# Optimization experiments

Measured on AMD Instinct MI355X. Metric: run time of the kernel, lower is better.

The kernel has to match this reference:

```python
import jax, jax.numpy as jnp
import numpy as np

D_MODEL = 1024
D_FF = 4096
N_EXPERTS = 8
TOP_K = 2
GATE_TEMP = 1.0
LOAD_BALANCE_WEIGHT = 0.01


def setup_inputs() -> dict:
    key = jax.random.key(0)
    ks = jax.random.split(key, 6)
    B, S = 4, 2048
    x = jax.random.normal(ks[0], (B, S, D_MODEL), dtype=jnp.float32)
    # gate: nn.Linear(d_model, n_experts, bias=False), weight ~ N(0, 0.1)
    gate_w = 0.1 * jax.random.normal(ks[1], (N_EXPERTS, D_MODEL), dtype=jnp.float32)
    # stacked expert weights (stored as [in, out] for x @ W)
    s1 = 1.0 / np.sqrt(D_MODEL)
    s2 = 1.0 / np.sqrt(D_FF)
    W1 = jax.random.uniform(ks[2], (N_EXPERTS, D_MODEL, D_FF), jnp.float32, -s1, s1)
    b1 = jax.random.uniform(ks[3], (N_EXPERTS, D_FF), jnp.float32, -s1, s1)
    W2 = jax.random.uniform(ks[4], (N_EXPERTS, D_FF, D_MODEL), jnp.float32, -s2, s2)
    b2 = jax.random.uniform(ks[5], (N_EXPERTS, D_MODEL), jnp.float32, -s2, s2)
    return {"x": x, "gate_w": gate_w, "W1": W1, "b1": b1, "W2": W2, "b2": b2}


def reference(x, gate_w, W1, b1, W2, b2):
    B, S, D = x.shape
    E = gate_w.shape[0]
    xf = x.reshape(-1, D)                                  # [N, D]
    logits = (xf @ gate_w.T) / GATE_TEMP                   # [N, E]
    gate_probs = jax.nn.softmax(logits, axis=-1)           # [N, E]
    topk_probs, topk_idx = jax.lax.top_k(gate_probs, TOP_K)
    topk_probs = topk_probs / jnp.sum(topk_probs, axis=-1, keepdims=True)
    # per-token combine weight for each expert: [N, E]
    combine = jnp.einsum("nk,nke->ne", topk_probs,
                         jax.nn.one_hot(topk_idx, E, dtype=xf.dtype))
    out = jnp.zeros_like(xf)
    for e in range(E):  # fixed small loop over experts (structurally distinct weights)
        h = jax.nn.gelu(xf @ W1[e] + b1[e], approximate=False)  # [N, d_ff]
        out = out + combine[:, e:e + 1] * (h @ W2[e] + b2[e])
    out = out.reshape(B, S, D)
    # auxiliary load-balance loss (faithful: softmax probs > 0 almost surely)
    prob_mean = jnp.mean(gate_probs, axis=0)
    tokens_per_expert = jnp.mean((gate_probs > 0).astype(xf.dtype), axis=0)
    aux_loss = jnp.sum(prob_mean * tokens_per_expert) * E * LOAD_BALANCE_WEIGHT
    return out, aux_loss
```

## Files before the change

### kernel.cpp

```cpp
#include <hip/hip_runtime.h>
#include <cstdint>

typedef unsigned short u16;
typedef __attribute__((ext_vector_type(8))) __bf16 bf16x8;
typedef __attribute__((ext_vector_type(4))) float f32x4;

#define NTOK 8192
#define DM   1024
#define DFF  4096
#define NE   8
#define NT_MAX 136

typedef const __attribute__((address_space(1))) unsigned gl_u32;
typedef __attribute__((address_space(3))) unsigned lds_u32;

static __device__ __forceinline__ u16 f2bf(float f) {
    union { float f; unsigned u; } v; v.f = f;
    unsigned r = v.u + 0x7fffu + ((v.u >> 16) & 1u);
    return (u16)(r >> 16);
}

__global__ __launch_bounds__(256) void transpose_cvt_kernel(const float* __restrict__ W,
                                                            u16* __restrict__ WT,
                                                            int K, int F) {
    __shared__ float tile[32][33];
    size_t eo = (size_t)blockIdx.z * K * F;
    const float* src = W + eo;
    u16* dst = WT + eo;
    int f0 = blockIdx.x * 32, k0 = blockIdx.y * 32;
    int c = threadIdx.x & 31, r0 = threadIdx.x >> 5;
#pragma unroll
    for (int r = r0; r < 32; r += 8)
        tile[r][c] = src[(size_t)(k0 + r) * F + f0 + c];
    __syncthreads();
#pragma unroll
    for (int r = r0; r < 32; r += 8)
        dst[(size_t)(f0 + r) * K + k0 + c] = f2bf(tile[c][r]);
}

__global__ __launch_bounds__(256) void gate_kernel(const float* __restrict__ x,
                                                   const float* __restrict__ gw,
                                                   u16* __restrict__ xb,
                                                   int* __restrict__ cnt,
                                                   float* __restrict__ psum,
                                                   float* __restrict__ indsum,
                                                   int* __restrict__ list,
                                                   float* __restrict__ wgt,
                                                   int4* __restrict__ tokIE,
                                                   float2* __restrict__ tokW) {
    __shared__ float s_psum[NE], s_ind[NE];
    __shared__ int s_cnt[NE], s_base[NE];
    __shared__ int s_tok[NE][32];
    __shared__ float s_wgt[NE][32];
    __shared__ int s_e1[32], s_p1[32], s_e2[32], s_p2[32];
    __shared__ float s_w1[32], s_w2[32];
    int tid = threadIdx.x, lane = tid & 63, wid = tid >> 6;
    if (tid < NE) { s_psum[tid] = 0.f; s_ind[tid] = 0.f; s_cnt[tid] = 0; }
    __syncthreads();
#pragma unroll 1
    for (int it = 0; it < 8; it++) {
        int t = blockIdx.x * 32 + wid * 8 + it;
        const float* xr = x + (size_t)t * DM;
        float xv[16];
#pragma unroll
        for (int i = 0; i < 4; i++) {
            f32x4 v = *(const f32x4*)(xr + i * 256 + lane * 4);
            xv[4 * i + 0] = v[0]; xv[4 * i + 1] = v[1];
            xv[4 * i + 2] = v[2]; xv[4 * i + 3] = v[3];
            ushort4 o;
            o.x = f2bf(v[0]); o.y = f2bf(v[1]); o.z = f2bf(v[2]); o.w = f2bf(v[3]);
            *(ushort4*)(xb + (size_t)t * DM + i * 256 + lane * 4) = o;
        }
        float p[NE];
#pragma unroll
        for (int e = 0; e < NE; e++) {
            const float* gr = gw + (size_t)e * DM;
            float d = 0.f;
#pragma unroll
            for (int i = 0; i < 4; i++) {
                f32x4 g = *(const f32x4*)(gr + i * 256 + lane * 4);
                d += xv[4 * i] * g[0] + xv[4 * i + 1] * g[1]
                   + xv[4 * i + 2] * g[2] + xv[4 * i + 3] * g[3];
            }
#pragma unroll
            for (int off = 32; off; off >>= 1) d += __shfl_xor(d, off);
            p[e] = d;
        }
        float m = p[0];
#pragma unroll
        for (int e = 1; e < NE; e++) m = fmaxf(m, p[e]);
        float s = 0.f;
#pragma unroll
        for (int e = 0; e < NE; e++) { p[e] = expf(p[e] - m); s += p[e]; }
        float inv = 1.f / s;
#pragma unroll
        for (int e = 0; e < NE; e++) p[e] *= inv;
        int i1 = 0; float p1 = p[0];
#pragma unroll
        for (int e = 1; e < NE; e++) if (p[e] > p1) { p1 = p[e]; i1 = e; }
        int i2 = (i1 == 0) ? 1 : 0; float p2 = p[i2];
#pragma unroll
        for (int e = 0; e < NE; e++) if (e != i1 && p[e] > p2) { p2 = p[e]; i2 = e; }
        float wnorm = 1.f / (p1 + p2);
        if (lane == 0) {
#pragma unroll
            for (int e = 0; e < NE; e++) {
                atomicAdd(&s_psum[e], p[e]);
                atomicAdd(&s_ind[e], (p[e] > 0.f) ? 1.f : 0.f);
            }
            int pos1 = atomicAdd(&s_cnt[i1], 1);
            s_tok[i1][pos1] = t; s_wgt[i1][pos1] = p1 * wnorm;
            int pos2 = atomicAdd(&s_cnt[i2], 1);
            s_tok[i2][pos2] = t; s_wgt[i2][pos2] = p2 * wnorm;
            int sl = wid * 8 + it;
            s_e1[sl] = i1; s_p1[sl] = pos1; s_w1[sl] = p1 * wnorm;
            s_e2[sl] = i2; s_p2[sl] = pos2; s_w2[sl] = p2 * wnorm;
        }
    }
    __syncthreads();
    if (tid < NE) {
        s_base[tid] = atomicAdd(&cnt[tid], s_cnt[tid]);
        atomicAdd(&psum[tid], s_psum[tid]);
        atomicAdd(&indsum[tid], s_ind[tid]);
    }
    __syncthreads();
    for (int idx = tid; idx < NE * 32; idx += 256) {
        int e = idx >> 5, j = idx & 31;
        if (j < s_cnt[e]) {
            list[e * NTOK + s_base[e] + j] = s_tok[e][j];
            wgt[e * NTOK + s_base[e] + j] = s_wgt[e][j];
        }
    }
    if (tid < 32) {
        int t = blockIdx.x * 32 + tid;
        int e1 = s_e1[tid], e2 = s_e2[tid];
        tokIE[t] = make_int4(e1, s_base[e1] + s_p1[tid], e2, s_base[e2] + s_p2[tid]);
        tokW[t] = make_float2(s_w1[tid], s_w2[tid]);
    }
}

__global__ void finalize_kernel(const float* __restrict__ psum,
                                const float* __restrict__ indsum,
                                const int* __restrict__ cnt,
                                int* __restrict__ baseArr,
                                int* __restrict__ tileE,
                                int* __restrict__ tileM0,
                                int* __restrict__ nTiles,
                                float* __restrict__ out_aux) {
    if (threadIdx.x == 0) {
        float a = 0.f; int b = 0, nt = 0;
        for (int e = 0; e < NE; e++) {
            a += (psum[e] * (1.f / NTOK)) * (indsum[e] * (1.f / NTOK));
            baseArr[e] = b; b += cnt[e];
            int mt = (cnt[e] + 127) >> 7;
            for (int i = 0; i < mt; i++) { tileE[nt] = e; tileM0[nt] = i; nt++; }
        }
        nTiles[0] = nt;
        out_aux[0] = a * (float)NE * 0.01f;
    }
}

template <int KDIM, int EPI>
__global__ __launch_bounds__(256, 4) void gemm_kernel(const u16* __restrict__ A,
                                                      const u16* __restrict__ BT,
                                                      const float* __restrict__ bias,
                                                      const int* __restrict__ list,
                                                      const float* __restrict__ wgt,
                                                      const int* __restrict__ cnt,
                                                      const int* __restrict__ base,
                                                      const int* __restrict__ tileE,
                                                      const int* __restrict__ tileM0,
                                                      const int* __restrict__ nTiles,
                                                      u16* __restrict__ h_out,
                                                      float* __restrict__ out) {
    constexpr int NCOL = (EPI == 1) ? DFF : DM;
    constexpr int NY = NCOL / 128;
    constexpr int NT = KDIM / 64;
    constexpr int BAND = 4 * NY;
    int nwg = gridDim.x;
    int q = nwg >> 3, r = nwg & 7;
    int xcd = blockIdx.x & 7, idx0 = blockIdx.x >> 3;
    int wg = (xcd < r ? xcd * (q + 1) : r * (q + 1) + (xcd - r) * q) + idx0;
    int band = wg / BAND, ib = wg - band * BAND;
    int ny = ib >> 2;
    int t = band * 4 + (ib & 3);
    if (t >= nTiles[0]) return;
    int e = tileE[t];
    int m0 = tileM0[t] << 7;
    int M = cnt[e];
    int hb = base[e];
    int n0 = ny * 128;
    const int* le = list + e * NTOK;
    const float* we = wgt + e * NTOK;
    const u16* Bte = BT + (size_t)e * NCOL * KDIM;
    const float* be = bias + (size_t)e * NCOL;

    __shared__ __attribute__((aligned(16))) u16 lA[128 * 64];
    __shared__ __attribute__((aligned(16))) u16 lB[128 * 64];

    int tid = threadIdx.x;
    int lane = tid & 63, wid = tid >> 6;
    int wr = wid >> 1, wc = wid & 1;
    int r16 = lane & 15, hi = lane >> 4;
    int r8 = r16 & 7;

    const u16* aG[4]; const u16* bG[4]; int lofs[4];
#pragma unroll
    for (int qq = 0; qq < 4; qq++) {
        int lin = qq * 256 + tid;
        int row = lin >> 3, j = lin & 7;
        int js = j ^ (row & 7);
        lofs[qq] = lin * 8;
        int pos = m0 + row; if (pos > M - 1) pos = M - 1;
        size_t arow = (EPI == 1) ? (size_t)le[pos] : (size_t)(hb + pos);
        aG[qq] = A + arow * KDIM + js * 8;
        bG[qq] = Bte + (size_t)(n0 + row) * KDIM + js * 8;
    }

#define STAGE(k0)                                                                   \
    do {                                                                            \
        _Pragma("unroll")                                                           \
        for (int qq = 0; qq < 4; qq++) {                                            \
            __builtin_amdgcn_global_load_lds((gl_u32*)(aG[qq] + (k0)),              \
                (lds_u32*)(lA + lofs[qq]), 16, 0, 0);                               \
            __builtin_amdgcn_global_load_lds((gl_u32*)(bG[qq] + (k0)),              \
                (lds_u32*)(lB + lofs[qq]), 16, 0, 0);                               \
        }                                                                           \
    } while (0)

    f32x4 acc[4][4];
#pragma unroll
    for (int m = 0; m < 4; m++)
#pragma unroll
        for (int n = 0; n < 4; n++) acc[m][n] = (f32x4){0.f, 0.f, 0.f, 0.f};

    STAGE(0);

#pragma unroll 1
    for (int tI = 0; tI < NT; ++tI) {
        asm volatile("s_waitcnt vmcnt(0)" ::: "memory");
        __builtin_amdgcn_s_barrier();
#pragma unroll
        for (int kk = 0; kk < 2; kk++) {
            bf16x8 aF[4], bF[4];
            int ch = ((kk << 2) | hi) ^ r8;
#pragma unroll
            for (int m = 0; m < 4; m++)
                aF[m] = *(const bf16x8*)(lA + ((wr * 64 + m * 16 + r16) << 6) + (ch << 3));
#pragma unroll
            for (int n = 0; n < 4; n++)
                bF[n] = *(const bf16x8*)(lB + ((wc * 64 + n * 16 + r16) << 6) + (ch << 3));
            __builtin_amdgcn_s_setprio(1);
#pragma unroll
            for (int m = 0; m < 4; m++)
#pragma unroll
                for (int n = 0; n < 4; n++)
                    acc[m][n] = __builtin_amdgcn_mfma_f32_16x16x32_bf16(aF[m], bF[n], acc[m][n], 0, 0, 0);
            __builtin_amdgcn_s_setprio(0);
        }
        asm volatile("s_waitcnt lgkmcnt(0)" ::: "memory");
        __builtin_amdgcn_s_barrier();
        if (tI + 1 < NT) STAGE((tI + 1) * 64);
    }
#undef STAGE

#pragma unroll
    for (int m = 0; m < 4; m++) {
        int pr = m0 + wr * 64 + m * 16 + hi * 4;
#pragma unroll
        for (int n = 0; n < 4; n++) {
            int f = n0 + wc * 64 + n * 16 + r16;
#pragma unroll
            for (int j = 0; j < 4; j++) {
                int p = pr + j;
                if (p < M) {
                    if constexpr (EPI == 1) {
                        float v = acc[m][n][j] + be[f];
                        float ex = __expf(v * (1.5957691216f + 0.0713548162f * v * v));
                        v = v - v / (ex + 1.0f);
                        h_out[(size_t)(hb + p) * DFF + f] = f2bf(v);
                    } else if constexpr (EPI == 2) {
                        out[(size_t)(hb + p) * DM + f] = acc[m][n][j];
                    } else {
                        atomicAdd(out + (size_t)le[p] * DM + f,
                                  we[p] * (acc[m][n][j] + be[f]));
                    }
                }
            }
        }
    }
}

__global__ __launch_bounds__(256) void combine_kernel(const float* __restrict__ pairOut,
                                                      const float* __restrict__ b2,
                                                      const int4* __restrict__ tokIE,
                                                      const float2* __restrict__ tokW,
                                                      const int* __restrict__ baseArr,
                                                      float* __restrict__ out) {
    int t = blockIdx.x;
    int c = threadIdx.x * 4;
    int4 ie = tokIE[t];
    float2 w = tokW[t];
    int s1 = baseArr[ie.x] + ie.y, s2 = baseArr[ie.z] + ie.w;
    f32x4 v1 = *(const f32x4*)(pairOut + (size_t)s1 * DM + c);
    f32x4 v2 = *(const f32x4*)(pairOut + (size_t)s2 * DM + c);
    f32x4 g1 = *(const f32x4*)(b2 + (size_t)ie.x * DM + c);
    f32x4 g2 = *(const f32x4*)(b2 + (size_t)ie.z * DM + c);
    f32x4 res = w.x * (v1 + g1) + w.y * (v2 + g2);
    *(f32x4*)(out + (size_t)t * DM + c) = res;
}

extern "C" void kernel_launch(void* const* d_in, const int* in_sizes, int n_in,
                              void* d_out, int out_size, void* d_ws, size_t ws_size,
                              hipStream_t stream) {
    const float* x  = (const float*)d_in[0];
    const float* gw = (const float*)d_in[1];
    const float* W1 = (const float*)d_in[2];
    const float* b1 = (const float*)d_in[3];
    const float* W2 = (const float*)d_in[4];
    const float* b2 = (const float*)d_in[5];
    float* out = (float*)d_out;

    char* ws = (char*)d_ws;
    size_t o_xb   = 0;
    size_t o_w1t  = (size_t)16 << 20;
    size_t o_w2t  = o_w1t + ((size_t)64 << 20);
    size_t o_h    = o_w2t + ((size_t)64 << 20);
    size_t o_pair = o_h + ((size_t)128 << 20);
    size_t ctrl_sz = (size_t)1 << 20;
    bool pair_path = ws_size >= o_pair + ((size_t)64 << 20) + ctrl_sz;
    size_t o_ctrl = pair_path ? (o_pair + ((size_t)64 << 20)) : o_pair;

    u16* xb   = (u16*)(ws + o_xb);
    u16* w1t  = (u16*)(ws + o_w1t);
    u16* w2t  = (u16*)(ws + o_w2t);
    u16* h    = (u16*)(ws + o_h);
    float* pairOut = (float*)(ws + o_pair);
    char* ctrl = ws + o_ctrl;
    int*    cnt     = (int*)ctrl;
    float*  psum    = (float*)(ctrl + 32);
    float*  indsum  = (float*)(ctrl + 64);
    int*    baseArr = (int*)(ctrl + 96);
    int*    list    = (int*)(ctrl + 192);
    float*  wgt     = (float*)(ctrl + 192 + 262144);
    int4*   tokIE   = (int4*)(ctrl + 192 + 524288);
    float2* tokW    = (float2*)(ctrl + 192 + 655360);
    int*    tileE   = (int*)(ctrl + 192 + 720896);
    int*    tileM0  = (int*)(ctrl + 192 + 724992);
    int*    nTiles  = (int*)(ctrl + 192 + 729088);

    (void)hipMemsetAsync(ctrl, 0, 192, stream);
    if (!pair_path)
        (void)hipMemsetAsync(d_out, 0, (size_t)out_size * sizeof(float), stream);

    transpose_cvt_kernel<<<dim3(DFF / 32, DM / 32, NE), 256, 0, stream>>>(W1, w1t, DM, DFF);
    transpose_cvt_kernel<<<dim3(DM / 32, DFF / 32, NE), 256, 0, stream>>>(W2, w2t, DFF, DM);
    gate_kernel<<<NTOK / 32, 256, 0, stream>>>(x, gw, xb, cnt, psum, indsum, list, wgt, tokIE, tokW);
    finalize_kernel<<<1, 64, 0, stream>>>(psum, indsum, cnt, baseArr, tileE, tileM0, nTiles,
                                          out + (size_t)NTOK * DM);

    gemm_kernel<DM, 1><<<dim3(NT_MAX * (DFF / 128)), 256, 0, stream>>>(
        xb, w1t, b1, list, wgt, cnt, baseArr, tileE, tileM0, nTiles, h, nullptr);
    if (pair_path) {
        gemm_kernel<DFF, 2><<<dim3(NT_MAX * (DM / 128)), 256, 0, stream>>>(
            h, w2t, b2, list, wgt, cnt, baseArr, tileE, tileM0, nTiles, nullptr, pairOut);
        combine_kernel<<<NTOK, 256, 0, stream>>>(pairOut, b2, tokIE, tokW, baseArr, out);
    } else {
        gemm_kernel<DFF, 3><<<dim3(NT_MAX * (DM / 128)), 256, 0, stream>>>(
            h, w2t, b2, list, wgt, cnt, baseArr, tileE, tileM0, nTiles, nullptr, out);
    }
}
```

Baseline: 572.3 us.

## Grow expert GEMM tiles to 256x128 with 512-thread blocks; vectorize weight transpose

The grouped expert GEMMs now use 256-row M tiles computed by 8 waves of 512 threads. Each B tile loaded into LDS is shared by twice as many rows, which halves weight traffic per output. The tile count per expert and the grid bound are recomputed to match. The weight transpose/convert kernel now reads with float4 vectors and writes 16-byte bf16 chunks on a 64x32 tile. Larger tiles waste more padding rows for experts with ragged counts, and they lower occupancy per CU.

Measured after the change: 572.6 us. Within noise of the previous version (+0.1%).

```diff
diff --git a/kernel.cpp b/kernel.cpp
--- a/kernel.cpp
+++ b/kernel.cpp
@@ -9,7 +9,7 @@
 #define DM   1024
 #define DFF  4096
 #define NE   8
-#define NT_MAX 136
+#define NT_MAX256 72
 
 typedef const __attribute__((address_space(1))) unsigned gl_u32;
 typedef __attribute__((address_space(3))) unsigned lds_u32;
@@ -23,19 +23,31 @@
 __global__ __launch_bounds__(256) void transpose_cvt_kernel(const float* __restrict__ W,
                                                             u16* __restrict__ WT,
                                                             int K, int F) {
-    __shared__ float tile[32][33];
+    __shared__ float tile[64][33];
     size_t eo = (size_t)blockIdx.z * K * F;
     const float* src = W + eo;
     u16* dst = WT + eo;
-    int f0 = blockIdx.x * 32, k0 = blockIdx.y * 32;
-    int c = threadIdx.x & 31, r0 = threadIdx.x >> 5;
-#pragma unroll
-    for (int r = r0; r < 32; r += 8)
-        tile[r][c] = src[(size_t)(k0 + r) * F + f0 + c];
+    int k0 = blockIdx.y * 64, f0 = blockIdx.x * 32;
+    int tid = threadIdx.x;
+    {
+        int rk = tid >> 2, cf = (tid & 3) * 8;
+        const float* s = src + (size_t)(k0 + rk) * F + f0 + cf;
+        f32x4 v0 = *(const f32x4*)(s);
+        f32x4 v1 = *(const f32x4*)(s + 4);
+#pragma unroll
+        for (int i = 0; i < 4; i++) { tile[rk][cf + i] = v0[i]; tile[rk][cf + 4 + i] = v1[i]; }
+    }
     __syncthreads();
-#pragma unroll
-    for (int r = r0; r < 32; r += 8)
-        dst[(size_t)(f0 + r) * K + k0 + c] = f2bf(tile[c][r]);
+    {
+        int f = tid >> 3, kq = (tid & 7) * 8;
+        union { ushort4 h[2]; uint4 q; } o;
+#pragma unroll
+        for (int i = 0; i < 8; i++) {
+            u16 b = f2bf(tile[kq + i][f]);
+            ((u16*)&o)[i] = b;
+        }
+        *(uint4*)(dst + (size_t)(f0 + f) * K + k0 + kq) = o.q;
+    }
 }
 
 __global__ __launch_bounds__(256) void gate_kernel(const float* __restrict__ x,
@@ -152,7 +164,7 @@
         for (int e = 0; e < NE; e++) {
             a += (psum[e] * (1.f / NTOK)) * (indsum[e] * (1.f / NTOK));
             baseArr[e] = b; b += cnt[e];
-            int mt = (cnt[e] + 127) >> 7;
+            int mt = (cnt[e] + 255) >> 8;
             for (int i = 0; i < mt; i++) { tileE[nt] = e; tileM0[nt] = i; nt++; }
         }
         nTiles[0] = nt;
@@ -161,7 +173,7 @@
 }
 
 template <int KDIM, int EPI>
-__global__ __launch_bounds__(256, 4) void gemm_kernel(const u16* __restrict__ A,
+__global__ __launch_bounds__(512, 2) void gemm_kernel(const u16* __restrict__ A,
                                                       const u16* __restrict__ BT,
                                                       const float* __restrict__ bias,
                                                       const int* __restrict__ list,
@@ -186,7 +198,7 @@
     int t = band * 4 + (ib & 3);
     if (t >= nTiles[0]) return;
     int e = tileE[t];
-    int m0 = tileM0[t] << 7;
+    int m0 = tileM0[t] << 8;
     int M = cnt[e];
     int hb = base[e];
     int n0 = ny * 128;
@@ -195,37 +207,45 @@
     const u16* Bte = BT + (size_t)e * NCOL * KDIM;
     const float* be = bias + (size_t)e * NCOL;
 
-    __shared__ __attribute__((aligned(16))) u16 lA[128 * 64];
+    __shared__ __attribute__((aligned(16))) u16 lA[256 * 64];
     __shared__ __attribute__((aligned(16))) u16 lB[128 * 64];
 
     int tid = threadIdx.x;
     int lane = tid & 63, wid = tid >> 6;
-    int wr = wid >> 1, wc = wid & 1;
+    int wm = wid >> 1, wn = wid & 1;
     int r16 = lane & 15, hi = lane >> 4;
     int r8 = r16 & 7;
 
-    const u16* aG[4]; const u16* bG[4]; int lofs[4];
+    const u16* aG[4]; const u16* bG[2]; int aOfs[4], bOfs[2];
 #pragma unroll
     for (int qq = 0; qq < 4; qq++) {
-        int lin = qq * 256 + tid;
+        int lin = qq * 512 + tid;
         int row = lin >> 3, j = lin & 7;
         int js = j ^ (row & 7);
-        lofs[qq] = lin * 8;
+        aOfs[qq] = lin * 8;
         int pos = m0 + row; if (pos > M - 1) pos = M - 1;
         size_t arow = (EPI == 1) ? (size_t)le[pos] : (size_t)(hb + pos);
         aG[qq] = A + arow * KDIM + js * 8;
+    }
+#pragma unroll
+    for (int qq = 0; qq < 2; qq++) {
+        int lin = qq * 512 + tid;
+        int row = lin >> 3, j = lin & 7;
+        int js = j ^ (row & 7);
+        bOfs[qq] = lin * 8;
         bG[qq] = Bte + (size_t)(n0 + row) * KDIM + js * 8;
     }
 
 #define STAGE(k0)                                                                   \
     do {                                                                            \
         _Pragma("unroll")                                                           \
-        for (int qq = 0; qq < 4; qq++) {                                            \
+        for (int qq = 0; qq < 4; qq++)                                              \
             __builtin_amdgcn_global_load_lds((gl_u32*)(aG[qq] + (k0)),              \
-                (lds_u32*)(lA + lofs[qq]), 16, 0, 0);                               \
+                (lds_u32*)(lA + aOfs[qq]), 16, 0, 0);                               \
+        _Pragma("unroll")                                                           \
+        for (int qq = 0; qq < 2; qq++)                                              \
             __builtin_amdgcn_global_load_lds((gl_u32*)(bG[qq] + (k0)),              \
-                (lds_u32*)(lB + lofs[qq]), 16, 0, 0);                               \
-        }                                                                           \
+                (lds_u32*)(lB + bOfs[qq]), 16, 0, 0);                               \
     } while (0)
 
     f32x4 acc[4][4];
@@ -246,10 +266,10 @@
             int ch = ((kk << 2) | hi) ^ r8;
 #pragma unroll
             for (int m = 0; m < 4; m++)
-                aF[m] = *(const bf16x8*)(lA + ((wr * 64 + m * 16 + r16) << 6) + (ch << 3));
+                aF[m] = *(const bf16x8*)(lA + ((wm * 64 + m * 16 + r16) << 6) + (ch << 3));
 #pragma unroll
             for (int n = 0; n < 4; n++)
-                bF[n] = *(const bf16x8*)(lB + ((wc * 64 + n * 16 + r16) << 6) + (ch << 3));
+                bF[n] = *(const bf16x8*)(lB + ((wn * 64 + n * 16 + r16) << 6) + (ch << 3));
             __builtin_amdgcn_s_setprio(1);
 #pragma unroll
             for (int m = 0; m < 4; m++)
@@ -266,10 +286,10 @@
 
 #pragma unroll
     for (int m = 0; m < 4; m++) {
-        int pr = m0 + wr * 64 + m * 16 + hi * 4;
+        int pr = m0 + wm * 64 + m * 16 + hi * 4;
 #pragma unroll
         for (int n = 0; n < 4; n++) {
-            int f = n0 + wc * 64 + n * 16 + r16;
+            int f = n0 + wn * 64 + n * 16 + r16;
 #pragma unroll
             for (int j = 0; j < 4; j++) {
                 int p = pr + j;
@@ -353,20 +373,20 @@
     if (!pair_path)
         (void)hipMemsetAsync(d_out, 0, (size_t)out_size * sizeof(float), stream);
 
-    transpose_cvt_kernel<<<dim3(DFF / 32, DM / 32, NE), 256, 0, stream>>>(W1, w1t, DM, DFF);
-    transpose_cvt_kernel<<<dim3(DM / 32, DFF / 32, NE), 256, 0, stream>>>(W2, w2t, DFF, DM);
+    transpose_cvt_kernel<<<dim3(DFF / 32, DM / 64, NE), 256, 0, stream>>>(W1, w1t, DM, DFF);
+    transpose_cvt_kernel<<<dim3(DM / 32, DFF / 64, NE), 256, 0, stream>>>(W2, w2t, DFF, DM);
     gate_kernel<<<NTOK / 32, 256, 0, stream>>>(x, gw, xb, cnt, psum, indsum, list, wgt, tokIE, tokW);
     finalize_kernel<<<1, 64, 0, stream>>>(psum, indsum, cnt, baseArr, tileE, tileM0, nTiles,
                                           out + (size_t)NTOK * DM);
 
-    gemm_kernel<DM, 1><<<dim3(NT_MAX * (DFF / 128)), 256, 0, stream>>>(
+    gemm_kernel<DM, 1><<<dim3(NT_MAX256 * (DFF / 128)), 512, 0, stream>>>(
         xb, w1t, b1, list, wgt, cnt, baseArr, tileE, tileM0, nTiles, h, nullptr);
     if (pair_path) {
-        gemm_kernel<DFF, 2><<<dim3(NT_MAX * (DM / 128)), 256, 0, stream>>>(
+        gemm_kernel<DFF, 2><<<dim3(NT_MAX256 * (DM / 128)), 512, 0, stream>>>(
             h, w2t, b2, list, wgt, cnt, baseArr, tileE, tileM0, nTiles, nullptr, pairOut);
         combine_kernel<<<NTOK, 256, 0, stream>>>(pairOut, b2, tokIE, tokW, baseArr, out);
     } else {
-        gemm_kernel<DFF, 3><<<dim3(NT_MAX * (DM / 128)), 256, 0, stream>>>(
+        gemm_kernel<DFF, 3><<<dim3(NT_MAX256 * (DM / 128)), 512, 0, stream>>>(
             h, w2t, b2, list, wgt, cnt, baseArr, tileE, tileM0, nTiles, nullptr, out);
     }
 }
```
